# Optimization experiments

Measured on AMD Instinct MI355X. Metric: run time of the kernel, lower is better.

## Reference

```python
import jax, jax.numpy as jnp
import numpy as np

D_STATE = 8
D_CONV = 4
DT_RANK = 8
THRESHOLD = 0.5
KPOOL = 3
PAD = (KPOOL - 1) // 2
EPS = 1e-5


def _rmsnorm(x, w):
    return x * jax.lax.rsqrt(jnp.mean(x * x, axis=-1, keepdims=True) + EPS) * w


def _dw_causal_conv(x, w, b):
    # x: (L, T, C), w: (C, 1, K) depthwise causal conv along T
    xt = jnp.transpose(x, (0, 2, 1))  # (L, C, T)
    y = jax.lax.conv_general_dilated(
        xt, w, window_strides=(1,), padding=[(D_CONV - 1, 0)],
        dimension_numbers=('NCH', 'OIH', 'NCH'), feature_group_count=xt.shape[1])
    return jnp.transpose(y, (0, 2, 1)) + b


def _selective_scan(x, delta, A, B, Cm, D):
    # x, delta: (L,T,d); A: (d,n); B, Cm: (L,T,n); D: (d,)
    dA = jnp.exp(delta[..., None] * A)                        # (L,T,d,n)
    dBx = (delta * x)[..., None] * B[:, :, None, :]           # (L,T,d,n)
    def combine(a, b):
        a1, b1 = a
        a2, b2 = b
        return (a2 * a1, a2 * b1 + b2)
    _, h = jax.lax.associative_scan(combine, (dA, dBx), axis=1)
    y = jnp.einsum('ltdn,ltn->ltd', h, Cm)
    return y + x * D


def _mamba_block(x, in_proj, conv_w, conv_b, x_proj_w, dt_proj_w, dt_proj_b,
                 A_log_f, A_log_b, D_f, D_b, out_proj_w, rms_w):
    # single-depth bidirectional (bimamba-v2 style) block, expand=1, residual + RMSNorm
    res = x
    xn = _rmsnorm(x, rms_w)
    xz = xn @ in_proj                       # (L,T,2C)
    xi, z = jnp.split(xz, 2, axis=-1)
    xi = jax.nn.silu(_dw_causal_conv(xi, conv_w, conv_b))
    dbl = xi @ x_proj_w                     # (L,T,dt_rank+2*d_state)
    dt = dbl[..., :DT_RANK]
    Bm = dbl[..., DT_RANK:DT_RANK + D_STATE]
    Cm = dbl[..., DT_RANK + D_STATE:]
    delta = jax.nn.softplus(dt @ dt_proj_w + dt_proj_b)
    A_f = -jnp.exp(A_log_f)
    A_b = -jnp.exp(A_log_b)
    flip = lambda a: a[:, ::-1]
    y_f = _selective_scan(xi, delta, A_f, Bm, Cm, D_f)
    y_b = flip(_selective_scan(flip(xi), flip(delta), A_b, flip(Bm), flip(Cm), D_b))
    y = 0.5 * (y_f + y_b) * jax.nn.silu(z)  # if_devide_out -> average two directions
    return res + y @ out_proj_w


def reference(feats, in_proj, conv_w, conv_b, x_proj_w, dt_proj_w, dt_proj_b,
              A_log_f, A_log_b, D_f, D_b, out_proj_w, rms_w, mlp_w, mlp_b,
              record_len):
    N, C, H, W = feats.shape
    T = H * W
    rec = np.asarray(record_len)  # static ragged group sizes
    ends = np.cumsum(rec)
    starts = ends - rec
    masks = []
    for s0, L in zip(starts.tolist(), rec.tolist()):
        g = feats[s0:s0 + L]                       # (L,C,H,W)
        if L > 1:
            x = g.reshape(L, C, T).transpose(0, 2, 1)  # l c h w -> l (h w) c
            feat = _mamba_block(x, in_proj, conv_w, conv_b, x_proj_w, dt_proj_w,
                                dt_proj_b, A_log_f, A_log_b, D_f, D_b,
                                out_proj_w, rms_w)
            score = jax.nn.sigmoid(feat @ mlp_w + mlp_b)   # (L,T,1)
            ego = jnp.ones((1, T, 1), feats.dtype)
            bs = jnp.concatenate([ego, score[1:]], axis=0)
        else:
            bs = jnp.ones((1, T, 1), feats.dtype)
        bs = bs.transpose(0, 2, 1).reshape(L, 1, H, W)     # l (h w) c -> l c h w
        masks.append(jnp.where(bs > THRESHOLD, 1.0, 0.0).astype(feats.dtype))
    mask = jnp.concatenate(masks, axis=0)                  # (N,1,H,W)
    pooled = jax.lax.reduce_window(
        mask, -jnp.inf, jax.lax.max,
        window_dimensions=(1, 1, KPOOL, KPOOL), window_strides=(1, 1, 1, 1),
        padding=[(0, 0), (0, 0), (PAD, PAD), (PAD, PAD)])
    return pooled


def setup_inputs():
    key = jax.random.key(0)
    ks = jax.random.split(key, 8)
    C, H, W = 128, 96, 96
    record_len = np.array([2, 3, 1, 2, 4], dtype=np.int64)
    N = int(record_len.sum())
    s = 0.05
    A_log = jnp.log(jnp.broadcast_to(
        jnp.arange(1, D_STATE + 1, dtype=jnp.float32), (C, D_STATE)))
    return {
        'feats': jax.random.normal(ks[0], (N, C, H, W), jnp.float32),
        'in_proj': jax.random.normal(ks[1], (C, 2 * C), jnp.float32) * s,
        'conv_w': jax.random.normal(ks[2], (C, 1, D_CONV), jnp.float32) * s,
        'conv_b': jnp.zeros((C,), jnp.float32),
        'x_proj_w': jax.random.normal(ks[3], (C, DT_RANK + 2 * D_STATE), jnp.float32) * s,
        'dt_proj_w': jax.random.normal(ks[4], (DT_RANK, C), jnp.float32) * s,
        'dt_proj_b': jnp.full((C,), 0.1, jnp.float32),
        'A_log_f': A_log,
        'A_log_b': A_log,
        'D_f': jnp.ones((C,), jnp.float32),
        'D_b': jnp.ones((C,), jnp.float32),
        'out_proj_w': jax.random.normal(ks[5], (C, C), jnp.float32) * s,
        'rms_w': jnp.ones((C,), jnp.float32),
        'mlp_w': jax.random.normal(ks[6], (C, 1), jnp.float32) * s,
        'mlp_b': jnp.zeros((1,), jnp.float32),
        'record_len': jnp.asarray(record_len),
    }
```

## Files before the change

kernel.cpp:

```cpp
#include <hip/hip_runtime.h>
#include <cstdint>
#include <cstddef>

#define C_CH 128
#define T_TOK 9216
#define H_IMG 96
#define W_IMG 96
#define NSTATE 8

#define CHUNK 64
#define RHALO 32
#define REGION (CHUNK + 2 * RHALO)

#define ASTRIDE 68
#define XSTRIDE 129
#define AU_FLOATS 8704

__device__ __forceinline__ float siluf_dev(float x) {
  return x / (1.0f + expf(-x));
}

__device__ __forceinline__ float fast_silu(float x) {
  return __fdividef(x, 1.0f + __expf(-x));
}

__global__ __launch_bounds__(128) void k0_setup(
    const int* __restrict__ rec, int n_groups, int N,
    const float* __restrict__ out_proj_w, const float* __restrict__ mlp_w,
    float* __restrict__ vvec, int* __restrict__ slot)
{
  const int tid = threadIdx.x;
  if (tid == 0) {
    int f = 0, sl = 0;
    for (int g = 0; g < n_groups; ++g) {
      const int L = rec[g];
      slot[f] = -1;
      for (int i = 1; i < L; ++i) slot[f + i] = sl++;
      f += L;
    }
  }
  if (tid < C_CH) {
    float acc = 0.0f;
    for (int j = 0; j < C_CH; ++j) acc += out_proj_w[tid * C_CH + j] * mlp_w[j];
    vvec[tid] = acc;
  }
}

__global__ __launch_bounds__(256, 4) void k12_gemmproj(
    const float* __restrict__ feats, const float* __restrict__ in_proj,
    const float* __restrict__ rms_w, const float* __restrict__ mlp_w,
    const float* __restrict__ mlp_b, const float* __restrict__ vvec,
    const float* __restrict__ conv_w, const float* __restrict__ conv_b,
    const float* __restrict__ x_proj_w,
    const float* __restrict__ dt_proj_w, const float* __restrict__ dt_proj_b,
    const int* __restrict__ slot,
    float* __restrict__ wbuf, float* __restrict__ logit,
    float* __restrict__ xd_g, float* __restrict__ bc_g)
{
  __shared__ float Asm[AU_FLOATS];
  __shared__ float redA[256], redB[256];
  __shared__ float irS[68];
  __shared__ float haloA[12];
  __shared__ float dtb[64 * 8];
  const int f = blockIdx.y;
  const int s = slot[f];
  if (s < 0) return;
  const int m0 = blockIdx.x * 64;
  const int tid = threadIdx.x;
  const size_t rowbase = (size_t)s * T_TOK;

  {
    const int c0 = tid >> 4;
    const int tq = (tid & 15) * 4;
    const float* src = feats + (size_t)f * C_CH * T_TOK + m0 + tq;
    #pragma unroll
    for (int i = 0; i < 8; ++i) {
      const int c = c0 + i * 16;
      const float4 x4 = *(const float4*)(src + (size_t)c * T_TOK);
      *(float4*)&Asm[c * ASTRIDE + 4 + tq] = x4;
    }
  }
  if (m0 > 0 && tid < C_CH) {
    const float* src = feats + (size_t)f * C_CH * T_TOK + (size_t)tid * T_TOK + m0 - 3;
    Asm[tid * ASTRIDE + 0] = src[0];
    Asm[tid * ASTRIDE + 1] = src[1];
    Asm[tid * ASTRIDE + 2] = src[2];
  }
  __syncthreads();
  {
    const int t = tid & 63;
    const int q = tid >> 6;
    float ssum = 0.0f, rm = 0.0f;
    for (int cc = q * 32; cc < q * 32 + 32; ++cc) {
      const float val = Asm[cc * ASTRIDE + 4 + t];
      ssum += val * val;
      rm += val * mlp_w[cc];
    }
    redA[tid] = ssum; redB[tid] = rm;
    if (m0 > 0 && tid < 12) {
      const int j = tid >> 2, qh = tid & 3;
      float ss = 0.0f;
      for (int cc = qh * 32; cc < qh * 32 + 32; ++cc) {
        const float v = Asm[cc * ASTRIDE + j];
        ss += v * v;
      }
      haloA[tid] = ss;
    }
  }
  __syncthreads();
  if (tid < 64) {
    const int t = tid;
    const float ssum = redA[t] + redA[t + 64] + redA[t + 128] + redA[t + 192];
    const float rm   = redB[t] + redB[t + 64] + redB[t + 128] + redB[t + 192];
    const float ir = 1.0f / sqrtf(ssum * (1.0f / C_CH) + 1e-5f);
    logit[rowbase + m0 + t] = rm + mlp_b[0];
    irS[4 + t] = ir;
  } else if (m0 > 0 && tid < 67) {
    const int j = tid - 64;
    const float ss = haloA[j * 4] + haloA[j * 4 + 1] + haloA[j * 4 + 2] + haloA[j * 4 + 3];
    irS[j] = 1.0f / sqrtf(ss * (1.0f / C_CH) + 1e-5f);
  }
  __syncthreads();
  {
    const int t = tid & 63;
    const int q = tid >> 6;
    const float ir = irS[4 + t];
    for (int cc = q * 32; cc < q * 32 + 32; ++cc)
      Asm[cc * ASTRIDE + 4 + t] = (Asm[cc * ASTRIDE + 4 + t] * ir) * rms_w[cc];
    if (m0 > 0 && tid < 12) {
      const int j = tid >> 2, qh = tid & 3;
      const float irh = irS[j];
      for (int cc = qh * 32; cc < qh * 32 + 32; ++cc)
        Asm[cc * ASTRIDE + j] = (Asm[cc * ASTRIDE + j] * irh) * rms_w[cc];
    }
  }
  __syncthreads();

  const int ti = tid >> 4;
  const int tc = tid & 15;

#define GEMM_CHUNK(N0, ACC) do {                                              \
    const float* bp = in_proj + (N0) + tc * 4;                                \
    _Pragma("unroll 8")                                                       \
    for (int k = 0; k < C_CH; ++k) {                                          \
      const float4 a4 = *(const float4*)&Asm[k * ASTRIDE + 4 + ti * 4];       \
      const float4 b4 = *(const float4*)(bp + (size_t)k * 256);               \
      ACC[0][0] += a4.x * b4.x; ACC[0][1] += a4.x * b4.y; ACC[0][2] += a4.x * b4.z; ACC[0][3] += a4.x * b4.w; \
      ACC[1][0] += a4.y * b4.x; ACC[1][1] += a4.y * b4.y; ACC[1][2] += a4.y * b4.z; ACC[1][3] += a4.y * b4.w; \
      ACC[2][0] += a4.z * b4.x; ACC[2][1] += a4.z * b4.y; ACC[2][2] += a4.z * b4.z; ACC[2][3] += a4.z * b4.w; \
      ACC[3][0] += a4.w * b4.x; ACC[3][1] += a4.w * b4.y; ACC[3][2] += a4.w * b4.z; ACC[3][3] += a4.w * b4.w; \
    } } while (0)

  #pragma unroll
  for (int zc4 = 0; zc4 < 2; ++zc4) {
    float acc[4][4];
    #pragma unroll
    for (int i = 0; i < 4; ++i)
      #pragma unroll
      for (int j = 0; j < 4; ++j) acc[i][j] = 0.0f;
    GEMM_CHUNK(128 + zc4 * 64, acc);
    const int zc = zc4 * 64 + tc * 4;
    const float4 v4 = *(const float4*)&vvec[zc];
    #pragma unroll
    for (int i = 0; i < 4; ++i) {
      const int t = m0 + ti * 4 + i;
      float4 o;
      o.x = 0.5f * siluf_dev(acc[i][0]) * v4.x;
      o.y = 0.5f * siluf_dev(acc[i][1]) * v4.y;
      o.z = 0.5f * siluf_dev(acc[i][2]) * v4.z;
      o.w = 0.5f * siluf_dev(acc[i][3]) * v4.w;
      *(float4*)&wbuf[(rowbase + t) * C_CH + zc] = o;
    }
  }

  float acc0[4][4], acc1[4][4];
  #pragma unroll
  for (int i = 0; i < 4; ++i)
    #pragma unroll
    for (int j = 0; j < 4; ++j) { acc0[i][j] = 0.0f; acc1[i][j] = 0.0f; }
  GEMM_CHUNK(0, acc0);
  GEMM_CHUNK(64, acc1);
#undef GEMM_CHUNK

  float hx0 = 0.0f, hx1 = 0.0f;
  {
    const int j0 = tid >> 7;
    const int cc0 = tid & 127;
    if (m0 > 0) {
      for (int k = 0; k < C_CH; ++k) {
        const float b0v = in_proj[(size_t)k * 256 + cc0];
        hx0 += Asm[k * ASTRIDE + j0] * b0v;
        if (tid < 128) hx1 += Asm[k * ASTRIDE + 2] * in_proj[(size_t)k * 256 + tid];
      }
    }
  }
  __syncthreads();

  {
    #pragma unroll
    for (int i = 0; i < 4; ++i) {
      const int row = 3 + ti * 4 + i;
      #pragma unroll
      for (int j = 0; j < 4; ++j) {
        Asm[row * XSTRIDE + tc * 4 + j] = acc0[i][j];
        Asm[row * XSTRIDE + 64 + tc * 4 + j] = acc1[i][j];
      }
    }
    Asm[(tid >> 7) * XSTRIDE + (tid & 127)] = hx0;
    if (tid < 128) Asm[2 * XSTRIDE + tid] = hx1;
  }
  __syncthreads();

  const int c = tid & 127;
  const int half = tid >> 7;
  {
    const float4 cw = *(const float4*)(conv_w + c * 4);
    const float cb = conv_b[c];
    const int row0 = half ? 35 : 3;
    float xm1 = Asm[(row0 - 1) * XSTRIDE + c];
    float xm2 = Asm[(row0 - 2) * XSTRIDE + c];
    float xm3 = Asm[(row0 - 3) * XSTRIDE + c];
    __syncthreads();
    #pragma unroll
    for (int i = 0; i < 32; ++i) {
      const int row = row0 + i;
      const float cur = Asm[row * XSTRIDE + c];
      const float sum = cw.x * xm3 + cw.y * xm2 + cw.z * xm1 + cw.w * cur + cb;
      Asm[row * XSTRIDE + c] = fast_silu(sum);
      xm3 = xm2; xm2 = xm1; xm1 = cur;
    }
  }
  __syncthreads();

  {
    const int q6 = __builtin_amdgcn_readfirstlane(tid >> 6) * 6;
    const int tok = tid & 63;
    float acc[6] = {0, 0, 0, 0, 0, 0};
    for (int cc = 0; cc < C_CH; ++cc) {
      const float xv = Asm[(3 + tok) * XSTRIDE + cc];
      #pragma unroll
      for (int jj = 0; jj < 6; ++jj)
        acc[jj] += xv * x_proj_w[cc * 24 + q6 + jj];
    }
    #pragma unroll
    for (int jj = 0; jj < 6; ++jj) {
      const int o = q6 + jj;
      if (o < 8) dtb[tok * 8 + o] = acc[jj];
      else       bc_g[(rowbase + m0 + tok) * 16 + (o - 8)] = acc[jj];
    }
  }
  __syncthreads();

  {
    float dw[8];
    #pragma unroll
    for (int r = 0; r < 8; ++r) dw[r] = dt_proj_w[r * C_CH + c];
    const float bias = dt_proj_b[c];
    for (int i = 0; i < 32; ++i) {
      const int tok = half * 32 + i;
      const float4 d0 = *(const float4*)&dtb[tok * 8];
      const float4 d1 = *(const float4*)&dtb[tok * 8 + 4];
      float pre = bias;
      pre += d0.x * dw[0] + d0.y * dw[1] + d0.z * dw[2] + d0.w * dw[3];
      pre += d1.x * dw[4] + d1.y * dw[5] + d1.z * dw[6] + d1.w * dw[7];
      const float dlt = fmaxf(pre, 0.0f) + __logf(1.0f + __expf(-fabsf(pre)));
      float2 xd;
      xd.x = Asm[(3 + tok) * XSTRIDE + c];
      xd.y = dlt;
      *(float2*)&xd_g[(rowbase + m0 + tok) * (2 * C_CH) + c * 2] = xd;
    }
  }
}

__global__ __launch_bounds__(256, 4) void k3_scan(
    const float* __restrict__ xd_g, const float* __restrict__ wbuf,
    const float* __restrict__ bc_g,
    const float* __restrict__ A_log_f, const float* __restrict__ A_log_b,
    const float* __restrict__ D_f, const float* __restrict__ D_b,
    const int* __restrict__ slot, float* __restrict__ logit)
{
  __shared__ float bc[REGION * 16];
  const int f = blockIdx.y;
  const int s = slot[f];
  if (s < 0) return;
  const int c0 = blockIdx.x * CHUNK;
  const int r0 = c0 - RHALO;
  const int tid = threadIdx.x;
  const int c = tid & 127;
  const int half = tid >> 7;
  const size_t rowbase = (size_t)s * T_TOK;

  {
    const long grow = ((long)rowbase + r0) * 16;
    const int lo  = (r0 < 0) ? (-r0) * 4 : 0;
    const int hi  = (r0 + REGION > T_TOK) ? (T_TOK - r0) * 4 : REGION * 4;
    #pragma unroll
    for (int i = 0; i < 2; ++i) {
      const int idx = tid + i * 256;
      if (idx >= lo && idx < hi)
        *(float4*)&bc[idx * 4] = *(const float4*)&bc_g[grow + (long)idx * 4];
    }
  }
  __syncthreads();

  float Ac[8];
  const float* Alog = half ? A_log_b : A_log_f;
  #pragma unroll
  for (int n = 0; n < NSTATE; ++n) Ac[n] = -expf(Alog[c * NSTATE + n]);
  const float Dd = half ? D_b[c] : D_f[c];
  float h[8] = {0, 0, 0, 0, 0, 0, 0, 0};

  const float a0 = Ac[0];
  int okl = 1;
  #pragma unroll
  for (int n = 1; n < NSTATE; ++n)
    okl &= (fabsf(Ac[n] - (float)(n + 1) * a0) <= 1e-4f * fabsf(Ac[n])) ? 1 : 0;
  const bool fastA = (__all(okl) != 0);

  auto decay8 = [&](float dlt, float* dA) {
    if (fastA) {
      const float e1 = __expf(dlt * a0);
      const float e2 = e1 * e1, e3 = e2 * e1, e4 = e2 * e2;
      dA[0] = e1; dA[1] = e2; dA[2] = e3; dA[3] = e4;
      dA[4] = e4 * e1; dA[5] = e4 * e2; dA[6] = e4 * e3; dA[7] = e4 * e4;
    } else {
      #pragma unroll
      for (int n = 0; n < NSTATE; ++n) dA[n] = __expf(dlt * Ac[n]);
    }
  };

  if (half == 0) {
    const int tb = (r0 < 0) ? 0 : r0;
    const int outg0 = (c0 - tb) >> 3;
    const int ng = (c0 + CHUNK - tb) >> 3;
    for (int g = 0; g < ng; ++g) {
      const int t0 = tb + g * 8;
      const bool out = (g >= outg0);
      float xg[8], dg[8], wg[8];
      #pragma unroll
      for (int j = 0; j < 8; ++j) {
        const size_t r = rowbase + t0 + j;
        const float2 xd = *(const float2*)&xd_g[r * (2 * C_CH) + c * 2];
        xg[j] = xd.x;
        dg[j] = xd.y;
        wg[j] = out ? wbuf[r * C_CH + c] : 0.0f;
      }
      #pragma unroll
      for (int j = 0; j < 8; ++j) {
        const int t = t0 + j;
        const int p = t - r0;
        const float dlt = dg[j];
        const float xiv = xg[j];
        const float u = dlt * xiv;
        const float4 b0 = *(const float4*)&bc[p * 16];
        const float4 b1 = *(const float4*)&bc[p * 16 + 4];
        float dA[8];
        decay8(dlt, dA);
        h[0] = dA[0] * h[0] + u * b0.x;
        h[1] = dA[1] * h[1] + u * b0.y;
        h[2] = dA[2] * h[2] + u * b0.z;
        h[3] = dA[3] * h[3] + u * b0.w;
        h[4] = dA[4] * h[4] + u * b1.x;
        h[5] = dA[5] * h[5] + u * b1.y;
        h[6] = dA[6] * h[6] + u * b1.z;
        h[7] = dA[7] * h[7] + u * b1.w;
        if (out) {
          const float4 cc0 = *(const float4*)&bc[p * 16 + 8];
          const float4 cc1 = *(const float4*)&bc[p * 16 + 12];
          float y = xiv * Dd;
          y += h[0] * cc0.x + h[1] * cc0.y + h[2] * cc0.z + h[3] * cc0.w;
          y += h[4] * cc1.x + h[5] * cc1.y + h[6] * cc1.z + h[7] * cc1.w;
          float contrib = y * wg[j];
          contrib += __shfl_xor(contrib, 1);
          contrib += __shfl_xor(contrib, 2);
          contrib += __shfl_xor(contrib, 4);
          contrib += __shfl_xor(contrib, 8);
          contrib += __shfl_xor(contrib, 16);
          contrib += __shfl_xor(contrib, 32);
          if ((tid & 63) == 0) atomicAdd(&logit[rowbase + t], contrib);
        }
      }
    }
  } else {
    const int te2e = r0 + REGION;
    const int te2 = (te2e > T_TOK) ? T_TOK : te2e;
    const int outg0 = (te2 - (c0 + CHUNK)) >> 3;
    const int ng = (te2 - c0) >> 3;
    for (int g = 0; g < ng; ++g) {
      const int t0 = te2 - 1 - g * 8;
      const bool out = (g >= outg0);
      float xg[8], dg[8], wg[8];
      #pragma unroll
      for (int j = 0; j < 8; ++j) {
        const size_t r = rowbase + t0 - j;
        const float2 xd = *(const float2*)&xd_g[r * (2 * C_CH) + c * 2];
        xg[j] = xd.x;
        dg[j] = xd.y;
        wg[j] = out ? wbuf[r * C_CH + c] : 0.0f;
      }
      #pragma unroll
      for (int j = 0; j < 8; ++j) {
        const int t = t0 - j;
        const int p = t - r0;
        const float dlt = dg[j];
        const float xiv = xg[j];
        const float u = dlt * xiv;
        const float4 b0 = *(const float4*)&bc[p * 16];
        const float4 b1 = *(const float4*)&bc[p * 16 + 4];
        float dA[8];
        decay8(dlt, dA);
        h[0] = dA[0] * h[0] + u * b0.x;
        h[1] = dA[1] * h[1] + u * b0.y;
        h[2] = dA[2] * h[2] + u * b0.z;
        h[3] = dA[3] * h[3] + u * b0.w;
        h[4] = dA[4] * h[4] + u * b1.x;
        h[5] = dA[5] * h[5] + u * b1.y;
        h[6] = dA[6] * h[6] + u * b1.z;
        h[7] = dA[7] * h[7] + u * b1.w;
        if (out) {
          const float4 cc0 = *(const float4*)&bc[p * 16 + 8];
          const float4 cc1 = *(const float4*)&bc[p * 16 + 12];
          float y = xiv * Dd;
          y += h[0] * cc0.x + h[1] * cc0.y + h[2] * cc0.z + h[3] * cc0.w;
          y += h[4] * cc1.x + h[5] * cc1.y + h[6] * cc1.z + h[7] * cc1.w;
          float contrib = y * wg[j];
          contrib += __shfl_xor(contrib, 1);
          contrib += __shfl_xor(contrib, 2);
          contrib += __shfl_xor(contrib, 4);
          contrib += __shfl_xor(contrib, 8);
          contrib += __shfl_xor(contrib, 16);
          contrib += __shfl_xor(contrib, 32);
          if ((tid & 63) == 0) atomicAdd(&logit[rowbase + t], contrib);
        }
      }
    }
  }
}

__global__ __launch_bounds__(128) void k4_pool(
    const float* __restrict__ logit, const int* __restrict__ slot,
    float* __restrict__ out)
{
  const int w = threadIdx.x;
  if (w >= W_IMG) return;
  const int hh = blockIdx.x;
  const int f = blockIdx.y;
  const int s = slot[f];
  float m = 0.0f;
  if (s < 0) {
    m = 1.0f;
  } else {
    for (int dh = -1; dh <= 1; ++dh) {
      const int h2 = hh + dh;
      if (h2 < 0 || h2 >= H_IMG) continue;
      for (int dw = -1; dw <= 1; ++dw) {
        const int w2 = w + dw;
        if (w2 < 0 || w2 >= W_IMG) continue;
        if (logit[(size_t)s * T_TOK + h2 * W_IMG + w2] > 0.0f) m = 1.0f;
      }
    }
  }
  out[(size_t)f * T_TOK + hh * W_IMG + w] = m;
}

extern "C" void kernel_launch(void* const* d_in, const int* in_sizes, int n_in,
                              void* d_out, int out_size, void* d_ws, size_t ws_size,
                              hipStream_t stream) {
  const float* feats      = (const float*)d_in[0];
  const float* in_proj    = (const float*)d_in[1];
  const float* conv_w     = (const float*)d_in[2];
  const float* conv_b     = (const float*)d_in[3];
  const float* x_proj_w   = (const float*)d_in[4];
  const float* dt_proj_w  = (const float*)d_in[5];
  const float* dt_proj_b  = (const float*)d_in[6];
  const float* A_log_f    = (const float*)d_in[7];
  const float* A_log_b    = (const float*)d_in[8];
  const float* D_f        = (const float*)d_in[9];
  const float* D_b        = (const float*)d_in[10];
  const float* out_proj_w = (const float*)d_in[11];
  const float* rms_w      = (const float*)d_in[12];
  const float* mlp_w      = (const float*)d_in[13];
  const float* mlp_b      = (const float*)d_in[14];
  const int*   rec        = (const int*)d_in[15];

  const int N = in_sizes[0] / (C_CH * T_TOK);
  const int n_groups = in_sizes[15];
  int S = N - n_groups;
  if (S < 1) S = 1;

  char* p = (char*)d_ws;
  float* vvec  = (float*)p; p += 1024;
  int*   slot  = (int*)p;   p += ((N * 4 + 255) / 256) * 256;
  float* logit = (float*)p; p += (size_t)S * T_TOK * 4;
  float* wA    = (float*)p; p += (size_t)S * T_TOK * C_CH * 4;
  float* xd    = (float*)p; p += (size_t)S * T_TOK * (2 * C_CH) * 4;
  float* bcg   = (float*)p; p += (size_t)S * T_TOK * 16 * 4;
  (void)ws_size; (void)n_in; (void)out_size;

  k0_setup<<<1, 128, 0, stream>>>(rec, n_groups, N, out_proj_w, mlp_w, vvec, slot);
  k12_gemmproj<<<dim3(T_TOK / 64, N), 256, 0, stream>>>(
      feats, in_proj, rms_w, mlp_w, mlp_b, vvec,
      conv_w, conv_b, x_proj_w, dt_proj_w, dt_proj_b, slot,
      wA, logit, xd, bcg);
  k3_scan<<<dim3(T_TOK / CHUNK, N), 256, 0, stream>>>(
      xd, wA, bcg, A_log_f, A_log_b, D_f, D_b, slot, logit);
  k4_pool<<<dim3(H_IMG, N), 128, 0, stream>>>(logit, slot, (float*)d_out);
}
```

Before: 314.1 us.

## Drop setup kernel, compute slots and out-mlp vector inline, shrink scan chunk

Removes the single-block setup kernel: each kernel now derives its slot index from record_len with a small loop, and the GEMM kernel recomputes the out_proj·mlp_w vector into shared memory per block. Separately, the scan chunk is halved to 32 tokens while keeping the 32-token halo, and the scan's launch bounds are raised to 8 blocks per SM. This saves one launch and its dependency, but each GEMM block redoes a 128x128 dot product, and the smaller chunk doubles the number of scan blocks and raises the share of recomputed halo work.

Measured after the change: 323.0 us. 1.03x slower.

```diff
diff --git a/kernel.cpp b/kernel.cpp
--- a/kernel.cpp
+++ b/kernel.cpp
@@ -8,7 +8,7 @@
 #define W_IMG 96
 #define NSTATE 8
 
-#define CHUNK 64
+#define CHUNK 32
 #define RHALO 32
 #define REGION (CHUNK + 2 * RHALO)
 
@@ -24,36 +24,26 @@
   return __fdividef(x, 1.0f + __expf(-x));
 }
 
-__global__ __launch_bounds__(128) void k0_setup(
-    const int* __restrict__ rec, int n_groups, int N,
-    const float* __restrict__ out_proj_w, const float* __restrict__ mlp_w,
-    float* __restrict__ vvec, int* __restrict__ slot)
-{
-  const int tid = threadIdx.x;
-  if (tid == 0) {
-    int f = 0, sl = 0;
-    for (int g = 0; g < n_groups; ++g) {
-      const int L = rec[g];
-      slot[f] = -1;
-      for (int i = 1; i < L; ++i) slot[f + i] = sl++;
-      f += L;
-    }
-  }
-  if (tid < C_CH) {
-    float acc = 0.0f;
-    for (int j = 0; j < C_CH; ++j) acc += out_proj_w[tid * C_CH + j] * mlp_w[j];
-    vvec[tid] = acc;
-  }
+__device__ __forceinline__ int slot_of(const int* __restrict__ rec,
+                                       int n_groups, int f) {
+  int base = 0, sl = 0;
+  for (int g = 0; g < n_groups; ++g) {
+    const int L = rec[g];
+    if (f < base + L) return (f == base) ? -1 : (sl + (f - base - 1));
+    sl += L - 1;
+    base += L;
+  }
+  return -1;
 }
 
 __global__ __launch_bounds__(256, 4) void k12_gemmproj(
     const float* __restrict__ feats, const float* __restrict__ in_proj,
     const float* __restrict__ rms_w, const float* __restrict__ mlp_w,
-    const float* __restrict__ mlp_b, const float* __restrict__ vvec,
+    const float* __restrict__ mlp_b, const float* __restrict__ out_proj_w,
     const float* __restrict__ conv_w, const float* __restrict__ conv_b,
     const float* __restrict__ x_proj_w,
     const float* __restrict__ dt_proj_w, const float* __restrict__ dt_proj_b,
-    const int* __restrict__ slot,
+    const int* __restrict__ rec, int n_groups,
     float* __restrict__ wbuf, float* __restrict__ logit,
     float* __restrict__ xd_g, float* __restrict__ bc_g)
 {
@@ -62,12 +52,19 @@
   __shared__ float irS[68];
   __shared__ float haloA[12];
   __shared__ float dtb[64 * 8];
+  __shared__ float vv[128];
   const int f = blockIdx.y;
-  const int s = slot[f];
+  const int s = slot_of(rec, n_groups, f);
   if (s < 0) return;
   const int m0 = blockIdx.x * 64;
   const int tid = threadIdx.x;
   const size_t rowbase = (size_t)s * T_TOK;
+
+  if (tid < C_CH) {
+    float a = 0.0f;
+    for (int j = 0; j < C_CH; ++j) a += out_proj_w[tid * C_CH + j] * mlp_w[j];
+    vv[tid] = a;
+  }
 
   {
     const int c0 = tid >> 4;
@@ -160,7 +157,7 @@
       for (int j = 0; j < 4; ++j) acc[i][j] = 0.0f;
     GEMM_CHUNK(128 + zc4 * 64, acc);
     const int zc = zc4 * 64 + tc * 4;
-    const float4 v4 = *(const float4*)&vvec[zc];
+    const float4 v4 = *(const float4*)&vv[zc];
     #pragma unroll
     for (int i = 0; i < 4; ++i) {
       const int t = m0 + ti * 4 + i;
@@ -272,16 +269,16 @@
   }
 }
 
-__global__ __launch_bounds__(256, 4) void k3_scan(
+__global__ __launch_bounds__(256, 8) void k3_scan(
     const float* __restrict__ xd_g, const float* __restrict__ wbuf,
     const float* __restrict__ bc_g,
     const float* __restrict__ A_log_f, const float* __restrict__ A_log_b,
     const float* __restrict__ D_f, const float* __restrict__ D_b,
-    const int* __restrict__ slot, float* __restrict__ logit)
+    const int* __restrict__ rec, int n_groups, float* __restrict__ logit)
 {
   __shared__ float bc[REGION * 16];
   const int f = blockIdx.y;
-  const int s = slot[f];
+  const int s = slot_of(rec, n_groups, f);
   if (s < 0) return;
   const int c0 = blockIdx.x * CHUNK;
   const int r0 = c0 - RHALO;
@@ -438,14 +435,14 @@
 }
 
 __global__ __launch_bounds__(128) void k4_pool(
-    const float* __restrict__ logit, const int* __restrict__ slot,
+    const float* __restrict__ logit, const int* __restrict__ rec, int n_groups,
     float* __restrict__ out)
 {
   const int w = threadIdx.x;
   if (w >= W_IMG) return;
   const int hh = blockIdx.x;
   const int f = blockIdx.y;
-  const int s = slot[f];
+  const int s = slot_of(rec, n_groups, f);
   float m = 0.0f;
   if (s < 0) {
     m = 1.0f;
@@ -489,20 +486,17 @@
   if (S < 1) S = 1;
 
   char* p = (char*)d_ws;
-  float* vvec  = (float*)p; p += 1024;
-  int*   slot  = (int*)p;   p += ((N * 4 + 255) / 256) * 256;
   float* logit = (float*)p; p += (size_t)S * T_TOK * 4;
   float* wA    = (float*)p; p += (size_t)S * T_TOK * C_CH * 4;
   float* xd    = (float*)p; p += (size_t)S * T_TOK * (2 * C_CH) * 4;
   float* bcg   = (float*)p; p += (size_t)S * T_TOK * 16 * 4;
   (void)ws_size; (void)n_in; (void)out_size;
 
-  k0_setup<<<1, 128, 0, stream>>>(rec, n_groups, N, out_proj_w, mlp_w, vvec, slot);
   k12_gemmproj<<<dim3(T_TOK / 64, N), 256, 0, stream>>>(
-      feats, in_proj, rms_w, mlp_w, mlp_b, vvec,
-      conv_w, conv_b, x_proj_w, dt_proj_w, dt_proj_b, slot,
+      feats, in_proj, rms_w, mlp_w, mlp_b, out_proj_w,
+      conv_w, conv_b, x_proj_w, dt_proj_w, dt_proj_b, rec, n_groups,
       wA, logit, xd, bcg);
   k3_scan<<<dim3(T_TOK / CHUNK, N), 256, 0, stream>>>(
-      xd, wA, bcg, A_log_f, A_log_b, D_f, D_b, slot, logit);
-  k4_pool<<<dim3(H_IMG, N), 128, 0, stream>>>(logit, slot, (float*)d_out);
-}
+      xd, wA, bcg, A_log_f, A_log_b, D_f, D_b, rec, n_groups, logit);
+  k4_pool<<<dim3(H_IMG, N), 128, 0, stream>>>(logit, rec, n_groups, (float*)d_out);
+}
```
